# Performance work log

Measured on AMD Instinct MI355X. Metric: run time of the kernel, lower is better.

## Reference

```python
import jax, jax.numpy as jnp
import numpy as np

VOCAB = 32000
EMBED_DIM = 1024
NUM_DELTAS = 4
NUM_TOKENS = 8192


def setup_inputs() -> dict:
    key = jax.random.key(0)
    k1, k2, k3, k4 = jax.random.split(key, 4)
    input_ids = jax.random.randint(k1, (NUM_TOKENS,), 0, VOCAB)
    # -1 routes to the base table, 0..NUM_DELTAS-1 to delta tables
    weight_indices = jax.random.randint(k2, (NUM_TOKENS,), -1, NUM_DELTAS)
    base_weight = jax.random.normal(k3, (VOCAB, EMBED_DIM), dtype=jnp.float32) * 0.02
    delta_weights = jax.random.normal(k4, (NUM_DELTAS, VOCAB, EMBED_DIM), dtype=jnp.float32) * 0.02
    return {
        "input_ids": input_ids,
        "weight_indices": weight_indices,
        "base_weight": base_weight,
        "delta_weights": delta_weights,
    }


def reference(input_ids, weight_indices, base_weight, delta_weights):
    # Per-token table routing: torch loops over unique(weight_indices) doing
    # masked embedding + scatter; equivalently each token gathers row
    # input_ids[t] from table weight_indices[t] (-1 => base table).
    base_emb = base_weight[input_ids]  # [N, D]
    safe_idx = jnp.maximum(weight_indices, 0)  # clamp -1 for safe gather
    delta_emb = delta_weights[safe_idx, input_ids]  # [N, D]
    use_base = (weight_indices == -1)[:, None]
    return jnp.where(use_base, base_emb, delta_emb)
```

## Files before the change

kernel.cpp:

```cpp
#include <hip/hip_runtime.h>


static constexpr int kVocab    = 32000;
static constexpr int kEmbedDim = 1024;

__global__ __launch_bounds__(256) void routed_embed_kernel(
    const int* __restrict__ input_ids,
    const int* __restrict__ weight_indices,
    const float* __restrict__ base_weight,
    const float* __restrict__ delta_weights,
    float* __restrict__ out) {
    const int t  = blockIdx.x;
    const int id = input_ids[t];
    const int wi = weight_indices[t];

    const float* src = (wi < 0)
        ? base_weight + (size_t)id * kEmbedDim
        : delta_weights + ((size_t)wi * kVocab + (size_t)id) * kEmbedDim;

    const float4* __restrict__ s4 = reinterpret_cast<const float4*>(src);
    float4* __restrict__ o4 =
        reinterpret_cast<float4*>(out + (size_t)t * kEmbedDim);

    o4[threadIdx.x] = s4[threadIdx.x];
}

extern "C" void kernel_launch(void* const* d_in, const int* in_sizes, int n_in,
                              void* d_out, int out_size, void* d_ws, size_t ws_size,
                              hipStream_t stream) {
    const int*   input_ids      = (const int*)d_in[0];
    const int*   weight_indices = (const int*)d_in[1];
    const float* base_weight    = (const float*)d_in[2];
    const float* delta_weights  = (const float*)d_in[3];
    float*       out            = (float*)d_out;

    const int num_tokens = in_sizes[0];

    routed_embed_kernel<<<num_tokens, 256, 0, stream>>>(
        input_ids, weight_indices, base_weight, delta_weights, out);
}
```

Before: 15.95 us.

## Process four tokens per wave with batched loads and nontemporal stores

Each wave now handles four tokens, loading their ids and routing indices as vector loads and issuing all sixteen 16-byte row loads before any store, which raises memory-level parallelism per thread. The grid shrinks to num_tokens/16 blocks, cutting block-launch and index-load overhead. Output stores use nontemporal hints to avoid polluting cache with write-only data. It assumes num_tokens is divisible by 16 and uses more registers per thread.

```diff
diff --git a/kernel.cpp b/kernel.cpp
--- a/kernel.cpp
+++ b/kernel.cpp
@@ -3,6 +3,9 @@
 
 static constexpr int kVocab    = 32000;
 static constexpr int kEmbedDim = 1024;
+
+typedef float f32x4 __attribute__((ext_vector_type(4)));
+typedef int   i32x4 __attribute__((ext_vector_type(4)));
 
 __global__ __launch_bounds__(256) void routed_embed_kernel(
     const int* __restrict__ input_ids,
@@ -10,19 +13,39 @@
     const float* __restrict__ base_weight,
     const float* __restrict__ delta_weights,
     float* __restrict__ out) {
-    const int t  = blockIdx.x;
-    const int id = input_ids[t];
-    const int wi = weight_indices[t];
+    const int wave = threadIdx.x >> 6;
+    const int lane = threadIdx.x & 63;
+    const int t0   = (blockIdx.x * 4 + wave) * 4;
 
-    const float* src = (wi < 0)
-        ? base_weight + (size_t)id * kEmbedDim
-        : delta_weights + ((size_t)wi * kVocab + (size_t)id) * kEmbedDim;
+    const i32x4 ids = *reinterpret_cast<const i32x4*>(input_ids + t0);
+    const i32x4 wis = *reinterpret_cast<const i32x4*>(weight_indices + t0);
 
-    const float4* __restrict__ s4 = reinterpret_cast<const float4*>(src);
-    float4* __restrict__ o4 =
-        reinterpret_cast<float4*>(out + (size_t)t * kEmbedDim);
+    const f32x4* __restrict__ s4[4];
+#pragma unroll
+    for (int k = 0; k < 4; ++k) {
+        const int id = ids[k];
+        const int wi = wis[k];
+        const float* src = (wi < 0)
+            ? base_weight + (size_t)id * kEmbedDim
+            : delta_weights + ((size_t)wi * kVocab + (size_t)id) * kEmbedDim;
+        s4[k] = reinterpret_cast<const f32x4*>(src);
+    }
 
-    o4[threadIdx.x] = s4[threadIdx.x];
+    f32x4 v[4][4];
+#pragma unroll
+    for (int k = 0; k < 4; ++k)
+#pragma unroll
+        for (int j = 0; j < 4; ++j)
+            v[k][j] = s4[k][lane + 64 * j];
+
+#pragma unroll
+    for (int k = 0; k < 4; ++k) {
+        f32x4* __restrict__ o4 =
+            reinterpret_cast<f32x4*>(out + (size_t)(t0 + k) * kEmbedDim);
+#pragma unroll
+        for (int j = 0; j < 4; ++j)
+            __builtin_nontemporal_store(v[k][j], &o4[lane + 64 * j]);
+    }
 }
 
 extern "C" void kernel_launch(void* const* d_in, const int* in_sizes, int n_in,
@@ -35,7 +58,8 @@
     float*       out            = (float*)d_out;
 
     const int num_tokens = in_sizes[0];
+    const int grid       = num_tokens / 16;
 
-    routed_embed_kernel<<<num_tokens, 256, 0, stream>>>(
+    routed_embed_kernel<<<grid, 256, 0, stream>>>(
         input_ids, weight_indices, base_weight, delta_weights, out);
 }
```

Result: faster. 14.30 us (-10.3%).
